# Performance work log

Measured on AMD Instinct MI355X. Metric: run time of the kernel, lower is better.

Reference implementation:

```python
import jax, jax.numpy as jnp
import numpy as np

EPS = 1e-5  # nn.BatchNorm2d default eps


def _cbs(x, w, g, b, m, v):
    # Conv(k=1, bias=False) + BatchNorm2d(inference) + SiLU
    y = jnp.einsum('bchw,oc->bohw', x, w)
    s = (g * jax.lax.rsqrt(v + EPS))[None, :, None, None]
    y = (y - m[None, :, None, None]) * s + b[None, :, None, None]
    return y * jax.nn.sigmoid(y)


def setup_inputs():
    key = jax.random.key(0)
    B, D, H, W = 1, 256, 80, 80
    C = D // 2
    ks = jax.random.split(key, 20)
    r = lambda i, shape, sc=1.0: jax.random.normal(ks[i], shape, dtype=jnp.float32) * sc
    oC, oD = jnp.ones((C,), jnp.float32), jnp.ones((D,), jnp.float32)
    zC, zD = jnp.zeros((C,), jnp.float32), jnp.zeros((D,), jnp.float32)
    return {
        'x': r(0, (B, D, H, W)),
        'w1': r(1, (C, D), 0.05), 'g1': oC, 'b1': zC, 'm1': zC, 'v1': oC,
        'w2': r(2, (D, C), 0.05), 'g2': oD, 'b2': zD, 'm2': zD, 'v2': oD,
        'w3': r(3, (D, C), 0.05), 'g3': oD, 'b3': zD, 'm3': zD, 'v3': oD,
        'wq': r(4, (C, C), 0.05), 'bq': r(5, (C,), 0.01),
        'wk': r(6, (C, C), 0.05), 'bk': r(7, (C,), 0.01),
        'wv': r(8, (C, C), 0.05), 'bv': r(9, (C,), 0.01),
        'wp': r(10, (C, C), 0.05), 'bp': r(11, (C,), 0.01),
        'rel_h': r(12, (1, C, H, 1)), 'rel_w': r(13, (1, C, 1, W)),
        'ef_h': r(14, (1, C, H, 1)), 'ef_w': r(15, (1, C, 1, W)),
    }


def reference(x, w1, g1, b1, m1, v1, w2, g2, b2, m2, v2, w3, g3, b3, m3, v3,
              wq, bq, wk, bk, wv, bv, wp, bp, rel_h, rel_w, ef_h, ef_w):
    x1 = _cbs(x, w1, g1, b1, m1, v1)            # [B, C, H, W]
    B, C, H, W = x1.shape
    HW = H * W
    proj = lambda w, b: (jnp.einsum('bchw,oc->bohw', x1, w)
                         + b[None, :, None, None]).reshape(B, C, HW)
    q = proj(wq, bq)
    k = proj(wk, bk)
    v = proj(wv, bv)
    p = proj(wp, bp)
    # content-content + content-position attention branch
    cp = (rel_h + rel_w).reshape(C, HW)          # [C, HW]
    cc = jnp.einsum('bci,bcj->bij', q, k)        # [B, HW, HW]
    cpos = jnp.einsum('ci,bcj->bij', cp, q)      # [B, HW, HW]
    attn = jax.nn.softmax(cc + cpos, axis=-1)
    # out1[b,c,i] = sum_j v[b,c,j] * attn[b,i,j]  (bmm(v, attn^T))
    out1 = jnp.einsum('bcj,bij->bci', v, attn).reshape(B, C, H, W)
    # extra positional branch (valid because B == 1)
    ef = (ef_h + ef_w).reshape(B, C, HW)         # [1, C, HW]
    ce = jnp.einsum('bci,bcj->bij', p, ef)       # [B, HW, HW]
    eng = jax.nn.softmax(ce, axis=-1)
    out2 = jnp.einsum('bcj,bij->bci', ef, eng).reshape(B, C, H, W)
    return x + _cbs(out1, w2, g2, b2, m2, v2) + _cbs(out2, w3, g3, b3, m3, v3)
```

## Files before the change

### kernel.cpp

```cpp
#include <hip/hip_runtime.h>


typedef unsigned short u16;
typedef __attribute__((ext_vector_type(8))) short bf16x8;
typedef __attribute__((ext_vector_type(4))) float f32x4;
typedef __attribute__((ext_vector_type(4))) unsigned int u32x4;

#define HW 6400
#define BN_EPS 1e-5f

__device__ __forceinline__ u16 f2b(float f) {
  unsigned u = __float_as_uint(f);
  u += 0x7fffu + ((u >> 16) & 1u);
  return (u16)(u >> 16);
}
__device__ __forceinline__ unsigned pack2(float a, float b) {
  return (unsigned)f2b(a) | ((unsigned)f2b(b) << 16);
}
__device__ __forceinline__ f32x4 MFMA(bf16x8 a, bf16x8 b, f32x4 c) {
  return __builtin_amdgcn_mfma_f32_16x16x32_bf16(a, b, c, 0, 0, 0);
}
__device__ __forceinline__ float silu_f(float y) {
  return y / (1.0f + __expf(-y));
}
__device__ __forceinline__ bf16x8 pack8(f32x4 lo, f32x4 hi, float sc) {
  union { bf16x8 v; uint4 u; } r;
  r.u.x = pack2(lo[0] * sc, lo[1] * sc);
  r.u.y = pack2(lo[2] * sc, lo[3] * sc);
  r.u.z = pack2(hi[0] * sc, hi[1] * sc);
  r.u.w = pack2(hi[2] * sc, hi[3] * sc);
  return r.v;
}
__device__ __forceinline__ void gload_lds16(const u16* src, u16* dst) {
  __builtin_amdgcn_global_load_lds(
      (const __attribute__((address_space(1))) void*)src,
      (__attribute__((address_space(3))) void*)dst, 16, 0, 0);
}

__global__ void prep_all(
    const float* __restrict__ rel_h, const float* __restrict__ rel_w,
    const float* __restrict__ ef_h, const float* __restrict__ ef_w,
    const float* __restrict__ w1, const float* __restrict__ g1, const float* __restrict__ b1,
    const float* __restrict__ m1, const float* __restrict__ v1,
    const float* __restrict__ w2, const float* __restrict__ g2, const float* __restrict__ b2,
    const float* __restrict__ m2, const float* __restrict__ v2,
    const float* __restrict__ w3, const float* __restrict__ g3, const float* __restrict__ b3,
    const float* __restrict__ m3, const float* __restrict__ v3,
    const float* __restrict__ wq, const float* __restrict__ bq,
    const float* __restrict__ wk, const float* __restrict__ bk,
    const float* __restrict__ wv, const float* __restrict__ bv,
    const float* __restrict__ wp, const float* __restrict__ bp,
    u16* __restrict__ LT,
    u16* __restrict__ w1b, float* __restrict__ b1e,
    u16* __restrict__ Wcat, float* __restrict__ bcat,
    u16* __restrict__ w2b, float* __restrict__ b2e,
    u16* __restrict__ w3b, float* __restrict__ b3e,
    u16* __restrict__ efhT, u16* __restrict__ efwT,
    u16* __restrict__ efhB, u16* __restrict__ efwB,
    u16* __restrict__ expA, u16* __restrict__ expB,
    float* __restrict__ lbuf)
{
  const int b = blockIdx.x;
  const int t = threadIdx.x;
  if (b < 80) {
    const int h = b;
    const int c0 = (t & 63) * 2;
    const float rh0 = rel_h[c0 * 80 + h], rh1 = rel_h[(c0 + 1) * 80 + h];
    for (int wcol = (t >> 6); wcol < 80; wcol += 4) {
      const int i = h * 80 + wcol;
      float rw0 = rel_w[c0 * 80 + wcol], rw1 = rel_w[(c0 + 1) * 80 + wcol];
      *(unsigned*)&LT[(size_t)i * 256 + 128 + c0] = pack2(rh0 + rw0, rh1 + rw1);
    }
  } else if (b < 144) {
    const int tid = (b - 80) * 256 + t;
    const int stride = 64 * 256;
    for (int idx = tid; idx < 128 * 256; idx += stride) {
      int o = idx >> 8;
      float s = g1[o] * rsqrtf(v1[o] + BN_EPS);
      w1b[idx] = f2b(w1[idx] * s);
    }
    for (int idx = tid; idx < 128; idx += stride) {
      float s = g1[idx] * rsqrtf(v1[idx] + BN_EPS);
      b1e[idx] = b1[idx] - m1[idx] * s;
    }
    for (int idx = tid; idx < 4 * 128 * 128; idx += stride) {
      int which = idx >> 14, r = idx & 16383;
      const float* src = which == 0 ? wq : which == 1 ? wk : which == 2 ? wv : wp;
      Wcat[idx] = f2b(src[r]);
    }
    for (int idx = tid; idx < 512; idx += stride) {
      int which = idx >> 7, r = idx & 127;
      const float* src = which == 0 ? bq : which == 1 ? bk : which == 2 ? bv : bp;
      bcat[idx] = src[r];
    }
    for (int idx = tid; idx < 256 * 128; idx += stride) {
      int o = idx >> 7;
      float s2 = g2[o] * rsqrtf(v2[o] + BN_EPS);
      w2b[idx] = f2b(w2[idx] * s2);
      float s3 = g3[o] * rsqrtf(v3[o] + BN_EPS);
      w3b[idx] = f2b(w3[idx] * s3);
    }
    for (int idx = tid; idx < 256; idx += stride) {
      float s2 = g2[idx] * rsqrtf(v2[idx] + BN_EPS);
      b2e[idx] = b2[idx] - m2[idx] * s2;
      float s3 = g3[idx] * rsqrtf(v3[idx] + BN_EPS);
      b3e[idx] = b3[idx] - m3[idx] * s3;
    }
    for (int idx = tid; idx < 80 * 128; idx += stride) {
      int hj = idx >> 7, c = idx & 127;
      efhT[idx] = f2b(ef_h[c * 80 + hj]);
      efwT[idx] = f2b(ef_w[c * 80 + hj]);
    }
    for (int idx = tid; idx < 128 * 96; idx += stride) {
      int c = idx / 96, hj = idx % 96;
      efhB[idx] = hj < 80 ? f2b(ef_h[c * 80 + hj]) : (u16)0;
      efwB[idx] = hj < 80 ? f2b(ef_w[c * 80 + hj]) : (u16)0;
    }
  } else {
    const int tid = (b - 144) * 256 + t;
    const int stride = 32 * 256;
    for (int idx = tid; idx < HW / 4; idx += stride)
      ((f32x4*)lbuf)[idx] = (f32x4){0.f, 0.f, 0.f, 0.f};
    for (int idx = tid; idx < HW * 96 / 8; idx += stride) {
      ((u32x4*)expA)[idx] = (u32x4){0, 0, 0, 0};
      ((u32x4*)expB)[idx] = (u32x4){0, 0, 0, 0};
    }
  }
}

__global__ __launch_bounds__(64) void front_k(
    const float* __restrict__ x,
    const u16* __restrict__ w1b, const float* __restrict__ b1e,
    const u16* __restrict__ Wcat, const float* __restrict__ bcat,
    u16* __restrict__ LT, u16* __restrict__ RT, u16* __restrict__ Vv,
    u16* __restrict__ pT)
{
  __shared__ __align__(16) float xs[16][260];
  __shared__ __align__(16) u16 tr[16][136];
  const int t = threadIdx.x, lane = t & 63, jl = lane & 15, q = lane >> 4;
  const int i0 = blockIdx.x * 16;

#pragma unroll
  for (int p = 0; p < 16; ++p) {
    const int ch = p * 16 + (lane >> 2);
    const int ii = (lane & 3) * 4;
    f32x4 v = *(const f32x4*)(x + (size_t)ch * HW + i0 + ii);
    xs[ii][ch] = v[0]; xs[ii + 1][ch] = v[1];
    xs[ii + 2][ch] = v[2]; xs[ii + 3][ch] = v[3];
  }
  __syncthreads();

  bf16x8 afr[8];
#pragma unroll
  for (int ks = 0; ks < 8; ++ks) {
    f32x4 va = *(const f32x4*)&xs[jl][ks * 32 + q * 8];
    f32x4 vb = *(const f32x4*)&xs[jl][ks * 32 + q * 8 + 4];
    afr[ks] = pack8(va, vb, 1.0f);
  }
  f32x4 acc[8];
#pragma unroll
  for (int nf = 0; nf < 8; ++nf) acc[nf] = (f32x4){0.f, 0.f, 0.f, 0.f};
#pragma unroll
  for (int ks = 0; ks < 8; ++ks)
#pragma unroll
    for (int nf = 0; nf < 8; ++nf) {
      bf16x8 b = *(const bf16x8*)(w1b + (size_t)(nf * 16 + jl) * 256 + ks * 32 + q * 8);
      acc[nf] = MFMA(afr[ks], b, acc[nf]);
    }
#pragma unroll
  for (int nf = 0; nf < 8; ++nf) {
    const int c = nf * 16 + jl;
    const float bias = b1e[c];
#pragma unroll
    for (int r = 0; r < 4; ++r)
      tr[q * 4 + r][c] = f2b(silu_f(acc[nf][r] + bias));
  }
  __syncthreads();
  bf16x8 xa[4];
#pragma unroll
  for (int ks = 0; ks < 4; ++ks)
    xa[ks] = *(const bf16x8*)&tr[jl][ks * 32 + q * 8];

#pragma unroll
  for (int nc = 0; nc < 4; ++nc) {
    f32x4 a2[8];
#pragma unroll
    for (int nf = 0; nf < 8; ++nf) a2[nf] = (f32x4){0.f, 0.f, 0.f, 0.f};
#pragma unroll
    for (int ks = 0; ks < 4; ++ks)
#pragma unroll
      for (int nf = 0; nf < 8; ++nf) {
        bf16x8 b = *(const bf16x8*)(Wcat + (size_t)(nc * 128 + nf * 16 + jl) * 128 + ks * 32 + q * 8);
        a2[nf] = MFMA(xa[ks], b, a2[nf]);
      }
    if (nc == 2) {
#pragma unroll
      for (int nf = 0; nf < 8; ++nf) {
        const int c = nf * 16 + jl;
        const float bias = bcat[256 + c];
        uint2 pk;
        pk.x = pack2(a2[nf][0] + bias, a2[nf][1] + bias);
        pk.y = pack2(a2[nf][2] + bias, a2[nf][3] + bias);
        *(uint2*)(Vv + (size_t)c * HW + i0 + q * 4) = pk;
      }
    } else {
      __syncthreads();
#pragma unroll
      for (int nf = 0; nf < 8; ++nf) {
        const int c = nf * 16 + jl;
        const float bias = bcat[nc * 128 + c];
#pragma unroll
        for (int r = 0; r < 4; ++r)
          tr[q * 4 + r][c] = f2b(a2[nf][r] + bias);
      }
      __syncthreads();
#pragma unroll
      for (int r = 0; r < 16; ++r) {
        unsigned val = *(const unsigned*)&tr[r][lane * 2];
        const size_t row = (size_t)(i0 + r);
        if (nc == 0) {
          *(unsigned*)(LT + row * 256 + lane * 2) = val;
          *(unsigned*)(RT + row * 256 + 128 + lane * 2) = val;
        } else if (nc == 1) {
          *(unsigned*)(RT + row * 256 + lane * 2) = val;
        } else {
          *(unsigned*)(pT + row * 128 + lane * 2) = val;
        }
      }
    }
  }
}

__global__ __launch_bounds__(256) void sep2a(
    const u16* __restrict__ pT,
    const u16* __restrict__ efhT,
    const u16* __restrict__ efwT,
    u16* __restrict__ expA, u16* __restrict__ expB,
    float* __restrict__ sA, float* __restrict__ sB)
{
  const int t = threadIdx.x, lane = t & 63, w = t >> 6, jl = lane & 15, q = lane >> 4;
  const int i0w = blockIdx.x * 128 + w * 32;

  bf16x8 pfr[2][4];
#pragma unroll
  for (int mt = 0; mt < 2; ++mt)
#pragma unroll
    for (int l = 0; l < 4; ++l)
      pfr[mt][l] = *(const bf16x8*)(pT + (size_t)(i0w + mt * 16 + jl) * 128 + l * 32 + q * 8);

  f32x4 sa[5][2], sb[5][2];
#pragma unroll
  for (int nf = 0; nf < 5; ++nf)
#pragma unroll
    for (int mt = 0; mt < 2; ++mt) {
      sa[nf][mt] = (f32x4){0.f, 0.f, 0.f, 0.f};
      sb[nf][mt] = (f32x4){0.f, 0.f, 0.f, 0.f};
    }
#pragma unroll
  for (int nf = 0; nf < 5; ++nf) {
    const int row = nf * 16 + jl;
#pragma unroll
    for (int l = 0; l < 4; ++l) {
      bf16x8 eh = *(const bf16x8*)(efhT + (size_t)row * 128 + l * 32 + q * 8);
      bf16x8 ew = *(const bf16x8*)(efwT + (size_t)row * 128 + l * 32 + q * 8);
      sa[nf][0] = MFMA(eh, pfr[0][l], sa[nf][0]);
      sa[nf][1] = MFMA(eh, pfr[1][l], sa[nf][1]);
      sb[nf][0] = MFMA(ew, pfr[0][l], sb[nf][0]);
      sb[nf][1] = MFMA(ew, pfr[1][l], sb[nf][1]);
    }
  }
#pragma unroll
  for (int mt = 0; mt < 2; ++mt) {
    const int i = i0w + mt * 16 + jl;
    float ra = 0.f, rb = 0.f;
#pragma unroll
    for (int nf = 0; nf < 5; ++nf) {
      float ea[4], eb[4];
#pragma unroll
      for (int r = 0; r < 4; ++r) {
        ea[r] = __expf(sa[nf][mt][r]); ra += ea[r];
        eb[r] = __expf(sb[nf][mt][r]); rb += eb[r];
      }
      uint2 pa, pb;
      pa.x = pack2(ea[0], ea[1]); pa.y = pack2(ea[2], ea[3]);
      pb.x = pack2(eb[0], eb[1]); pb.y = pack2(eb[2], eb[3]);
      *(uint2*)(expA + (size_t)i * 96 + nf * 16 + q * 4) = pa;
      *(uint2*)(expB + (size_t)i * 96 + nf * 16 + q * 4) = pb;
    }
    ra += __shfl_xor(ra, 16); ra += __shfl_xor(ra, 32);
    rb += __shfl_xor(rb, 16); rb += __shfl_xor(rb, 32);
    if (lane < 16) { sA[i] = ra; sB[i] = rb; }
  }
}

__global__ __launch_bounds__(512, 2) void fused_attn(
    const u16* __restrict__ LT,
    const u16* __restrict__ RT,
    const u16* __restrict__ Vv,
    float* __restrict__ Opart,
    float* __restrict__ lv)
{
  __shared__ __align__(1024) u16 Rs[2][128 * 128];
  __shared__ __align__(1024) u16 Ts[2][64 * 128];
  const int t = threadIdx.x, lane = t & 63, w = t >> 6, jl = lane & 15, q = lane >> 4;
  const int bid = blockIdx.x;
  const int jp = bid / 50, it = bid % 50;
  const int wi = w & 1, wj = w >> 1;
  const int i0w = it * 128 + wi * 64;
  u16* Tw = Ts[wi];

  bf16x8 afr[4][8];
#pragma unroll
  for (int mt = 0; mt < 4; ++mt)
#pragma unroll
    for (int l = 0; l < 8; ++l)
      afr[mt][l] = *(const bf16x8*)(LT + (size_t)(i0w + mt * 16 + jl) * 256 + l * 32 + q * 8);

  f32x4 o[4][2];
#pragma unroll
  for (int mt = 0; mt < 4; ++mt)
#pragma unroll
    for (int cf = 0; cf < 2; ++cf) o[mt][cf] = (f32x4){0.f, 0.f, 0.f, 0.f};
  float lacc[4] = {0.f, 0.f, 0.f, 0.f};

  auto stage = [&](int jj) {
#pragma unroll
    for (int k = 0; k < 8; ++k) {
      const int b = k >> 2, cl = k & 3;
      const int cc = w * 4 + cl;
      const int jr = cc * 4 + (lane >> 4);
      const int cp = lane & 15;
      const int ch = (cp & ~7) | ((cp ^ jr) & 7);
      gload_lds16(RT + (size_t)(jj + jr) * 256 + b * 128 + ch * 8,
                  Rs[b] + (cc << 9));
    }
  };

  stage(jp * 640);

  for (int stp = 0; stp < 5; ++stp) {
    const int jj = jp * 640 + stp * 128;

    f32x4 s[2][4];
#pragma unroll
    for (int nf = 0; nf < 2; ++nf)
#pragma unroll
      for (int mt = 0; mt < 4; ++mt) s[nf][mt] = (f32x4){0.f, 0.f, 0.f, 0.f};

    __syncthreads();

#pragma unroll
    for (int h = 0; h < 2; ++h)
#pragma unroll
      for (int nf = 0; nf < 2; ++nf) {
        const int row = wj * 32 + nf * 16 + jl;
#pragma unroll
        for (int l = 0; l < 4; ++l) {
          const int ch = (l * 4 + q) ^ (jl & 7);
          bf16x8 b = *(const bf16x8*)(Rs[h] + row * 128 + ch * 8);
          s[nf][0] = MFMA(b, afr[0][h * 4 + l], s[nf][0]);
          s[nf][1] = MFMA(b, afr[1][h * 4 + l], s[nf][1]);
          s[nf][2] = MFMA(b, afr[2][h * 4 + l], s[nf][2]);
          s[nf][3] = MFMA(b, afr[3][h * 4 + l], s[nf][3]);
        }
      }
    __syncthreads();
    if (stp < 4) stage(jj + 128);

#pragma unroll
    for (int nf = 0; nf < 2; ++nf)
#pragma unroll
      for (int mt = 0; mt < 4; ++mt)
#pragma unroll
        for (int r = 0; r < 4; ++r) {
          float p = __expf(s[nf][mt][r]);
          s[nf][mt][r] = p;
          lacc[mt] += p;
        }

#pragma unroll
    for (int mt = 0; mt < 4; ++mt)
#pragma unroll
      for (int nf = 0; nf < 2; ++nf) {
        const int row = mt * 16 + jl;
        const int cs = (wj * 8 + nf * 4 + q) ^ ((jl & 7) << 2);
        uint2 pk;
        pk.x = pack2(s[nf][mt][0], s[nf][mt][1]);
        pk.y = pack2(s[nf][mt][2], s[nf][mt][3]);
        *(uint2*)(Tw + row * 128 + cs * 4) = pk;
      }
    __syncthreads();

#pragma unroll
    for (int ks2 = 0; ks2 < 4; ++ks2) {
      bf16x8 bv0 = *(const bf16x8*)(Vv + (size_t)(wj * 32 + jl) * HW + jj + ks2 * 32 + q * 8);
      bf16x8 bv1 = *(const bf16x8*)(Vv + (size_t)(wj * 32 + 16 + jl) * HW + jj + ks2 * 32 + q * 8);
      const int cb = (ks2 * 8 + q * 2) ^ ((jl & 7) << 2);
#pragma unroll
      for (int mt = 0; mt < 4; ++mt) {
        bf16x8 pa = *(const bf16x8*)(Tw + (mt * 16 + jl) * 128 + cb * 4);
        o[mt][0] = MFMA(pa, bv0, o[mt][0]);
        o[mt][1] = MFMA(pa, bv1, o[mt][1]);
      }
    }
  }

#pragma unroll
  for (int mt = 0; mt < 4; ++mt) {
    float rsum = lacc[mt];
    rsum += __shfl_xor(rsum, 16);
    rsum += __shfl_xor(rsum, 32);
    if (lane < 16)
      atomicAdd(&lv[i0w + mt * 16 + jl], rsum);
  }
#pragma unroll
  for (int mt = 0; mt < 4; ++mt) {
    const int ib = i0w + mt * 16 + q * 4;
#pragma unroll
    for (int cf = 0; cf < 2; ++cf) {
      const int c = wj * 32 + cf * 16 + jl;
#pragma unroll
      for (int r = 0; r < 4; ++r)
        Opart[((size_t)(ib + r) * 10 + jp) * 128 + c] = o[mt][cf][r];
    }
  }
}

__global__ __launch_bounds__(256) void final2(
    const u16* __restrict__ expA, const u16* __restrict__ expB,
    const float* __restrict__ sA, const float* __restrict__ sB,
    const u16* __restrict__ efhB, const u16* __restrict__ efwB,
    const float* __restrict__ Opart,
    const float* __restrict__ lv,
    const u16* __restrict__ w2b, const float* __restrict__ b2e,
    const u16* __restrict__ w3b, const float* __restrict__ b3e,
    const float* __restrict__ x, float* __restrict__ outp)
{
  __shared__ __align__(16) u16 T2[64][136];
  const int t = threadIdx.x, lane = t & 63, w = t >> 6, jl = lane & 15, q = lane >> 4;
  const int i0 = blockIdx.x * 64;
  const int nc = blockIdx.y;
  const int rowA = i0 + w * 16 + jl;

  {
    bf16x8 fa[3], fb[3];
#pragma unroll
    for (int l = 0; l < 3; ++l) {
      fa[l] = *(const bf16x8*)(expA + (size_t)rowA * 96 + l * 32 + q * 8);
      fb[l] = *(const bf16x8*)(expB + (size_t)rowA * 96 + l * 32 + q * 8);
    }
    f32x4 oU[8], oW[8];
#pragma unroll
    for (int nf = 0; nf < 8; ++nf) {
      oU[nf] = (f32x4){0.f, 0.f, 0.f, 0.f};
      oW[nf] = (f32x4){0.f, 0.f, 0.f, 0.f};
    }
#pragma unroll
    for (int l = 0; l < 3; ++l)
#pragma unroll
      for (int nf = 0; nf < 8; ++nf) {
        bf16x8 bh = *(const bf16x8*)(efhB + (size_t)(nf * 16 + jl) * 96 + l * 32 + q * 8);
        bf16x8 bw = *(const bf16x8*)(efwB + (size_t)(nf * 16 + jl) * 96 + l * 32 + q * 8);
        oU[nf] = MFMA(fa[l], bh, oU[nf]);
        oW[nf] = MFMA(fb[l], bw, oW[nf]);
      }
    const int ib = i0 + w * 16 + q * 4;
    float ia[4], iw[4];
#pragma unroll
    for (int r = 0; r < 4; ++r) {
      ia[r] = 1.0f / sA[ib + r];
      iw[r] = 1.0f / sB[ib + r];
    }
#pragma unroll
    for (int nf = 0; nf < 8; ++nf)
#pragma unroll
      for (int r = 0; r < 4; ++r)
        T2[w * 16 + q * 4 + r][nf * 16 + jl] =
            f2b(oU[nf][r] * ia[r] + oW[nf][r] * iw[r]);
  }
  __syncthreads();

  const float inv1 = 1.0f / lv[rowA];
  const float* OrBase = Opart + (size_t)rowA * 10 * 128;
  f32x4 a1[8], a2[8];
#pragma unroll
  for (int nf = 0; nf < 8; ++nf) {
    a1[nf] = (f32x4){0.f, 0.f, 0.f, 0.f};
    a2[nf] = (f32x4){0.f, 0.f, 0.f, 0.f};
  }
#pragma unroll
  for (int ks = 0; ks < 4; ++ks) {
    f32x4 s1a = (f32x4){0.f, 0.f, 0.f, 0.f};
    f32x4 s1b = (f32x4){0.f, 0.f, 0.f, 0.f};
#pragma unroll
    for (int p = 0; p < 10; ++p) {
      const float* Or = OrBase + p * 128;
      s1a += *(const f32x4*)(Or + ks * 32 + q * 8);
      s1b += *(const f32x4*)(Or + ks * 32 + q * 8 + 4);
    }
    bf16x8 fa1 = pack8(s1a, s1b, inv1);
    bf16x8 fa2 = *(const bf16x8*)&T2[w * 16 + jl][ks * 32 + q * 8];
#pragma unroll
    for (int nf = 0; nf < 8; ++nf) {
      bf16x8 b2f = *(const bf16x8*)(w2b + (size_t)(nc * 128 + nf * 16 + jl) * 128 + ks * 32 + q * 8);
      bf16x8 b3f = *(const bf16x8*)(w3b + (size_t)(nc * 128 + nf * 16 + jl) * 128 + ks * 32 + q * 8);
      a1[nf] = MFMA(fa1, b2f, a1[nf]);
      a2[nf] = MFMA(fa2, b3f, a2[nf]);
    }
  }
#pragma unroll
  for (int nf = 0; nf < 8; ++nf) {
    const int d = nc * 128 + nf * 16 + jl;
    const float bb2 = b2e[d], bb3 = b3e[d];
    const size_t base = (size_t)d * HW + i0 + w * 16 + q * 4;
    f32x4 xv = *(const f32x4*)(x + base);
    f32x4 rv;
#pragma unroll
    for (int r = 0; r < 4; ++r)
      rv[r] = xv[r] + silu_f(a1[nf][r] + bb2) + silu_f(a2[nf][r] + bb3);
    *(f32x4*)(outp + base) = rv;
  }
}

extern "C" void kernel_launch(void* const* d_in, const int* in_sizes, int n_in,
                              void* d_out, int out_size, void* d_ws, size_t ws_size,
                              hipStream_t stream)
{
  (void)in_sizes; (void)n_in; (void)out_size; (void)ws_size;
  const float* x   = (const float*)d_in[0];
  const float* w1  = (const float*)d_in[1];
  const float* g1  = (const float*)d_in[2];
  const float* b1  = (const float*)d_in[3];
  const float* m1  = (const float*)d_in[4];
  const float* v1  = (const float*)d_in[5];
  const float* w2  = (const float*)d_in[6];
  const float* g2  = (const float*)d_in[7];
  const float* b2  = (const float*)d_in[8];
  const float* m2  = (const float*)d_in[9];
  const float* v2  = (const float*)d_in[10];
  const float* w3  = (const float*)d_in[11];
  const float* g3  = (const float*)d_in[12];
  const float* b3  = (const float*)d_in[13];
  const float* m3  = (const float*)d_in[14];
  const float* v3  = (const float*)d_in[15];
  const float* wq  = (const float*)d_in[16];
  const float* bq  = (const float*)d_in[17];
  const float* wk  = (const float*)d_in[18];
  const float* bk  = (const float*)d_in[19];
  const float* wv  = (const float*)d_in[20];
  const float* bv  = (const float*)d_in[21];
  const float* wp  = (const float*)d_in[22];
  const float* bp  = (const float*)d_in[23];
  const float* rel_h = (const float*)d_in[24];
  const float* rel_w = (const float*)d_in[25];
  const float* ef_h  = (const float*)d_in[26];
  const float* ef_w  = (const float*)d_in[27];
  float* outp = (float*)d_out;

  char* ws = (char*)d_ws;
  size_t off = 0;
  auto alloc = [&](size_t bytes) -> void* {
    void* p = ws + off;
    off += (bytes + 511) & ~(size_t)511;
    return p;
  };
  u16* LT    = (u16*)alloc((size_t)HW * 256 * 2);
  u16* RT    = (u16*)alloc((size_t)HW * 256 * 2);
  u16* pT    = (u16*)alloc((size_t)HW * 128 * 2);
  u16* Vv    = (u16*)alloc((size_t)HW * 128 * 2);
  float* Opart = (float*)alloc((size_t)HW * 10 * 128 * 4);
  float* lbuf  = (float*)alloc((size_t)HW * 4);
  u16* w1b   = (u16*)alloc(128 * 256 * 2);
  float* b1e = (float*)alloc(128 * 4);
  u16* Wcat  = (u16*)alloc(512 * 128 * 2);
  float* bcat = (float*)alloc(512 * 4);
  u16* w2b   = (u16*)alloc(256 * 128 * 2);
  float* b2e = (float*)alloc(256 * 4);
  u16* w3b   = (u16*)alloc(256 * 128 * 2);
  float* b3e = (float*)alloc(256 * 4);
  u16* efhT  = (u16*)alloc(80 * 128 * 2);
  u16* efwT  = (u16*)alloc(80 * 128 * 2);
  u16* efhB  = (u16*)alloc(128 * 96 * 2);
  u16* efwB  = (u16*)alloc(128 * 96 * 2);
  u16* expA  = (u16*)alloc((size_t)HW * 96 * 2);
  u16* expB  = (u16*)alloc((size_t)HW * 96 * 2);
  float* sA  = (float*)alloc(HW * 4);
  float* sB  = (float*)alloc(HW * 4);

  prep_all<<<176, 256, 0, stream>>>(rel_h, rel_w, ef_h, ef_w,
                                    w1, g1, b1, m1, v1, w2, g2, b2, m2, v2,
                                    w3, g3, b3, m3, v3, wq, bq, wk, bk, wv, bv, wp, bp,
                                    LT, w1b, b1e, Wcat, bcat, w2b, b2e, w3b, b3e,
                                    efhT, efwT, efhB, efwB, expA, expB, lbuf);
  front_k<<<400, 64, 0, stream>>>(x, w1b, b1e, Wcat, bcat, LT, RT, Vv, pT);
  sep2a<<<50, 256, 0, stream>>>(pT, efhT, efwT, expA, expB, sA, sB);
  fused_attn<<<500, 512, 0, stream>>>(LT, RT, Vv, Opart, lbuf);
  final2<<<dim3(100, 2), 256, 0, stream>>>(expA, expB, sA, sB, efhB, efwB,
                                           Opart, lbuf, w2b, b2e, w3b, b3e,
                                           x, outp);
}
```

Baseline: 245.2 us.

## Fuse ef-softmax kernel into final2 and spread front_k across four waves

Removes the sep2a kernel and its expA/expB/sA/sB global buffers: final2 now computes the p·ef scores, exponentials and row sums into shared memory for its 64-row tile before using them. This drops one launch, the zeroing of the exp buffers in prep_all, and a global write/read round trip. In exchange, the softmax work is repeated for each of the two blockIdx.y halves. Separately, front_k goes from one to four waves per block, each wave owning a quarter of the output columns and the load/store rows, to raise parallelism inside each block.

```diff
diff --git a/kernel.cpp b/kernel.cpp
--- a/kernel.cpp
+++ b/kernel.cpp
@@ -57,7 +57,6 @@
     u16* __restrict__ w3b, float* __restrict__ b3e,
     u16* __restrict__ efhT, u16* __restrict__ efwT,
     u16* __restrict__ efhB, u16* __restrict__ efwB,
-    u16* __restrict__ expA, u16* __restrict__ expB,
     float* __restrict__ lbuf)
 {
   const int b = blockIdx.x;
@@ -121,14 +120,10 @@
     const int stride = 32 * 256;
     for (int idx = tid; idx < HW / 4; idx += stride)
       ((f32x4*)lbuf)[idx] = (f32x4){0.f, 0.f, 0.f, 0.f};
-    for (int idx = tid; idx < HW * 96 / 8; idx += stride) {
-      ((u32x4*)expA)[idx] = (u32x4){0, 0, 0, 0};
-      ((u32x4*)expB)[idx] = (u32x4){0, 0, 0, 0};
-    }
-  }
-}
-
-__global__ __launch_bounds__(64) void front_k(
+  }
+}
+
+__global__ __launch_bounds__(256) void front_k(
     const float* __restrict__ x,
     const u16* __restrict__ w1b, const float* __restrict__ b1e,
     const u16* __restrict__ Wcat, const float* __restrict__ bcat,
@@ -137,11 +132,12 @@
 {
   __shared__ __align__(16) float xs[16][260];
   __shared__ __align__(16) u16 tr[16][136];
-  const int t = threadIdx.x, lane = t & 63, jl = lane & 15, q = lane >> 4;
+  const int t = threadIdx.x, lane = t & 63, w = t >> 6, jl = lane & 15, q = lane >> 4;
   const int i0 = blockIdx.x * 16;
 
 #pragma unroll
-  for (int p = 0; p < 16; ++p) {
+  for (int pp = 0; pp < 4; ++pp) {
+    const int p = w * 4 + pp;
     const int ch = p * 16 + (lane >> 2);
     const int ii = (lane & 3) * 4;
     f32x4 v = *(const f32x4*)(x + (size_t)ch * HW + i0 + ii);
@@ -157,23 +153,24 @@
     f32x4 vb = *(const f32x4*)&xs[jl][ks * 32 + q * 8 + 4];
     afr[ks] = pack8(va, vb, 1.0f);
   }
-  f32x4 acc[8];
-#pragma unroll
-  for (int nf = 0; nf < 8; ++nf) acc[nf] = (f32x4){0.f, 0.f, 0.f, 0.f};
+  f32x4 acc[2];
+#pragma unroll
+  for (int nn = 0; nn < 2; ++nn) acc[nn] = (f32x4){0.f, 0.f, 0.f, 0.f};
 #pragma unroll
   for (int ks = 0; ks < 8; ++ks)
 #pragma unroll
-    for (int nf = 0; nf < 8; ++nf) {
+    for (int nn = 0; nn < 2; ++nn) {
+      const int nf = w * 2 + nn;
       bf16x8 b = *(const bf16x8*)(w1b + (size_t)(nf * 16 + jl) * 256 + ks * 32 + q * 8);
-      acc[nf] = MFMA(afr[ks], b, acc[nf]);
-    }
-#pragma unroll
-  for (int nf = 0; nf < 8; ++nf) {
-    const int c = nf * 16 + jl;
+      acc[nn] = MFMA(afr[ks], b, acc[nn]);
+    }
+#pragma unroll
+  for (int nn = 0; nn < 2; ++nn) {
+    const int c = (w * 2 + nn) * 16 + jl;
     const float bias = b1e[c];
 #pragma unroll
     for (int r = 0; r < 4; ++r)
-      tr[q * 4 + r][c] = f2b(silu_f(acc[nf][r] + bias));
+      tr[q * 4 + r][c] = f2b(silu_f(acc[nn][r] + bias));
   }
   __syncthreads();
   bf16x8 xa[4];
@@ -183,39 +180,41 @@
 
 #pragma unroll
   for (int nc = 0; nc < 4; ++nc) {
-    f32x4 a2[8];
-#pragma unroll
-    for (int nf = 0; nf < 8; ++nf) a2[nf] = (f32x4){0.f, 0.f, 0.f, 0.f};
+    f32x4 a2[2];
+#pragma unroll
+    for (int nn = 0; nn < 2; ++nn) a2[nn] = (f32x4){0.f, 0.f, 0.f, 0.f};
 #pragma unroll
     for (int ks = 0; ks < 4; ++ks)
 #pragma unroll
-      for (int nf = 0; nf < 8; ++nf) {
+      for (int nn = 0; nn < 2; ++nn) {
+        const int nf = w * 2 + nn;
         bf16x8 b = *(const bf16x8*)(Wcat + (size_t)(nc * 128 + nf * 16 + jl) * 128 + ks * 32 + q * 8);
-        a2[nf] = MFMA(xa[ks], b, a2[nf]);
+        a2[nn] = MFMA(xa[ks], b, a2[nn]);
       }
     if (nc == 2) {
 #pragma unroll
-      for (int nf = 0; nf < 8; ++nf) {
-        const int c = nf * 16 + jl;
+      for (int nn = 0; nn < 2; ++nn) {
+        const int c = (w * 2 + nn) * 16 + jl;
         const float bias = bcat[256 + c];
         uint2 pk;
-        pk.x = pack2(a2[nf][0] + bias, a2[nf][1] + bias);
-        pk.y = pack2(a2[nf][2] + bias, a2[nf][3] + bias);
+        pk.x = pack2(a2[nn][0] + bias, a2[nn][1] + bias);
+        pk.y = pack2(a2[nn][2] + bias, a2[nn][3] + bias);
         *(uint2*)(Vv + (size_t)c * HW + i0 + q * 4) = pk;
       }
     } else {
       __syncthreads();
 #pragma unroll
-      for (int nf = 0; nf < 8; ++nf) {
-        const int c = nf * 16 + jl;
+      for (int nn = 0; nn < 2; ++nn) {
+        const int c = (w * 2 + nn) * 16 + jl;
         const float bias = bcat[nc * 128 + c];
 #pragma unroll
         for (int r = 0; r < 4; ++r)
-          tr[q * 4 + r][c] = f2b(a2[nf][r] + bias);
+          tr[q * 4 + r][c] = f2b(a2[nn][r] + bias);
       }
       __syncthreads();
 #pragma unroll
-      for (int r = 0; r < 16; ++r) {
+      for (int rr = 0; rr < 4; ++rr) {
+        const int r = w * 4 + rr;
         unsigned val = *(const unsigned*)&tr[r][lane * 2];
         const size_t row = (size_t)(i0 + r);
         if (nc == 0) {
@@ -228,68 +227,6 @@
         }
       }
     }
-  }
-}
-
-__global__ __launch_bounds__(256) void sep2a(
-    const u16* __restrict__ pT,
-    const u16* __restrict__ efhT,
-    const u16* __restrict__ efwT,
-    u16* __restrict__ expA, u16* __restrict__ expB,
-    float* __restrict__ sA, float* __restrict__ sB)
-{
-  const int t = threadIdx.x, lane = t & 63, w = t >> 6, jl = lane & 15, q = lane >> 4;
-  const int i0w = blockIdx.x * 128 + w * 32;
-
-  bf16x8 pfr[2][4];
-#pragma unroll
-  for (int mt = 0; mt < 2; ++mt)
-#pragma unroll
-    for (int l = 0; l < 4; ++l)
-      pfr[mt][l] = *(const bf16x8*)(pT + (size_t)(i0w + mt * 16 + jl) * 128 + l * 32 + q * 8);
-
-  f32x4 sa[5][2], sb[5][2];
-#pragma unroll
-  for (int nf = 0; nf < 5; ++nf)
-#pragma unroll
-    for (int mt = 0; mt < 2; ++mt) {
-      sa[nf][mt] = (f32x4){0.f, 0.f, 0.f, 0.f};
-      sb[nf][mt] = (f32x4){0.f, 0.f, 0.f, 0.f};
-    }
-#pragma unroll
-  for (int nf = 0; nf < 5; ++nf) {
-    const int row = nf * 16 + jl;
-#pragma unroll
-    for (int l = 0; l < 4; ++l) {
-      bf16x8 eh = *(const bf16x8*)(efhT + (size_t)row * 128 + l * 32 + q * 8);
-      bf16x8 ew = *(const bf16x8*)(efwT + (size_t)row * 128 + l * 32 + q * 8);
-      sa[nf][0] = MFMA(eh, pfr[0][l], sa[nf][0]);
-      sa[nf][1] = MFMA(eh, pfr[1][l], sa[nf][1]);
-      sb[nf][0] = MFMA(ew, pfr[0][l], sb[nf][0]);
-      sb[nf][1] = MFMA(ew, pfr[1][l], sb[nf][1]);
-    }
-  }
-#pragma unroll
-  for (int mt = 0; mt < 2; ++mt) {
-    const int i = i0w + mt * 16 + jl;
-    float ra = 0.f, rb = 0.f;
-#pragma unroll
-    for (int nf = 0; nf < 5; ++nf) {
-      float ea[4], eb[4];
-#pragma unroll
-      for (int r = 0; r < 4; ++r) {
-        ea[r] = __expf(sa[nf][mt][r]); ra += ea[r];
-        eb[r] = __expf(sb[nf][mt][r]); rb += eb[r];
-      }
-      uint2 pa, pb;
-      pa.x = pack2(ea[0], ea[1]); pa.y = pack2(ea[2], ea[3]);
-      pb.x = pack2(eb[0], eb[1]); pb.y = pack2(eb[2], eb[3]);
-      *(uint2*)(expA + (size_t)i * 96 + nf * 16 + q * 4) = pa;
-      *(uint2*)(expB + (size_t)i * 96 + nf * 16 + q * 4) = pb;
-    }
-    ra += __shfl_xor(ra, 16); ra += __shfl_xor(ra, 32);
-    rb += __shfl_xor(rb, 16); rb += __shfl_xor(rb, 32);
-    if (lane < 16) { sA[i] = ra; sB[i] = rb; }
   }
 }
 
@@ -427,8 +364,8 @@
 }
 
 __global__ __launch_bounds__(256) void final2(
-    const u16* __restrict__ expA, const u16* __restrict__ expB,
-    const float* __restrict__ sA, const float* __restrict__ sB,
+    const u16* __restrict__ pT,
+    const u16* __restrict__ efhT, const u16* __restrict__ efwT,
     const u16* __restrict__ efhB, const u16* __restrict__ efwB,
     const float* __restrict__ Opart,
     const float* __restrict__ lv,
@@ -436,18 +373,67 @@
     const u16* __restrict__ w3b, const float* __restrict__ b3e,
     const float* __restrict__ x, float* __restrict__ outp)
 {
+  __shared__ __align__(16) u16 eAs[64][104];
+  __shared__ __align__(16) u16 eBs[64][104];
+  __shared__ float sAL[64], sBL[64];
   __shared__ __align__(16) u16 T2[64][136];
   const int t = threadIdx.x, lane = t & 63, w = t >> 6, jl = lane & 15, q = lane >> 4;
   const int i0 = blockIdx.x * 64;
   const int nc = blockIdx.y;
   const int rowA = i0 + w * 16 + jl;
+  const int iloc = w * 16 + jl;
+
+  {
+    bf16x8 pfr[4];
+#pragma unroll
+    for (int l = 0; l < 4; ++l)
+      pfr[l] = *(const bf16x8*)(pT + (size_t)rowA * 128 + l * 32 + q * 8);
+    f32x4 sa[5], sb[5];
+#pragma unroll
+    for (int nf = 0; nf < 5; ++nf) {
+      sa[nf] = (f32x4){0.f, 0.f, 0.f, 0.f};
+      sb[nf] = (f32x4){0.f, 0.f, 0.f, 0.f};
+    }
+#pragma unroll
+    for (int nf = 0; nf < 5; ++nf) {
+      const int row = nf * 16 + jl;
+#pragma unroll
+      for (int l = 0; l < 4; ++l) {
+        bf16x8 eh = *(const bf16x8*)(efhT + (size_t)row * 128 + l * 32 + q * 8);
+        bf16x8 ew = *(const bf16x8*)(efwT + (size_t)row * 128 + l * 32 + q * 8);
+        sa[nf] = MFMA(eh, pfr[l], sa[nf]);
+        sb[nf] = MFMA(ew, pfr[l], sb[nf]);
+      }
+    }
+    float ra = 0.f, rb = 0.f;
+#pragma unroll
+    for (int nf = 0; nf < 5; ++nf) {
+      float ea[4], eb[4];
+#pragma unroll
+      for (int r = 0; r < 4; ++r) {
+        ea[r] = __expf(sa[nf][r]); ra += ea[r];
+        eb[r] = __expf(sb[nf][r]); rb += eb[r];
+      }
+      uint2 pa, pb;
+      pa.x = pack2(ea[0], ea[1]); pa.y = pack2(ea[2], ea[3]);
+      pb.x = pack2(eb[0], eb[1]); pb.y = pack2(eb[2], eb[3]);
+      *(uint2*)&eAs[iloc][nf * 16 + q * 4] = pa;
+      *(uint2*)&eBs[iloc][nf * 16 + q * 4] = pb;
+    }
+    *(uint2*)&eAs[iloc][80 + q * 4] = (uint2){0u, 0u};
+    *(uint2*)&eBs[iloc][80 + q * 4] = (uint2){0u, 0u};
+    ra += __shfl_xor(ra, 16); ra += __shfl_xor(ra, 32);
+    rb += __shfl_xor(rb, 16); rb += __shfl_xor(rb, 32);
+    if (lane < 16) { sAL[iloc] = ra; sBL[iloc] = rb; }
+  }
+  __syncthreads();
 
   {
     bf16x8 fa[3], fb[3];
 #pragma unroll
     for (int l = 0; l < 3; ++l) {
-      fa[l] = *(const bf16x8*)(expA + (size_t)rowA * 96 + l * 32 + q * 8);
-      fb[l] = *(const bf16x8*)(expB + (size_t)rowA * 96 + l * 32 + q * 8);
+      fa[l] = *(const bf16x8*)&eAs[iloc][l * 32 + q * 8];
+      fb[l] = *(const bf16x8*)&eBs[iloc][l * 32 + q * 8];
     }
     f32x4 oU[8], oW[8];
 #pragma unroll
@@ -464,12 +450,11 @@
         oU[nf] = MFMA(fa[l], bh, oU[nf]);
         oW[nf] = MFMA(fb[l], bw, oW[nf]);
       }
-    const int ib = i0 + w * 16 + q * 4;
     float ia[4], iw[4];
 #pragma unroll
     for (int r = 0; r < 4; ++r) {
-      ia[r] = 1.0f / sA[ib + r];
-      iw[r] = 1.0f / sB[ib + r];
+      ia[r] = 1.0f / sAL[w * 16 + q * 4 + r];
+      iw[r] = 1.0f / sBL[w * 16 + q * 4 + r];
     }
 #pragma unroll
     for (int nf = 0; nf < 8; ++nf)
@@ -582,20 +567,15 @@
   u16* efwT  = (u16*)alloc(80 * 128 * 2);
   u16* efhB  = (u16*)alloc(128 * 96 * 2);
   u16* efwB  = (u16*)alloc(128 * 96 * 2);
-  u16* expA  = (u16*)alloc((size_t)HW * 96 * 2);
-  u16* expB  = (u16*)alloc((size_t)HW * 96 * 2);
-  float* sA  = (float*)alloc(HW * 4);
-  float* sB  = (float*)alloc(HW * 4);
 
   prep_all<<<176, 256, 0, stream>>>(rel_h, rel_w, ef_h, ef_w,
                                     w1, g1, b1, m1, v1, w2, g2, b2, m2, v2,
                                     w3, g3, b3, m3, v3, wq, bq, wk, bk, wv, bv, wp, bp,
                                     LT, w1b, b1e, Wcat, bcat, w2b, b2e, w3b, b3e,
-                                    efhT, efwT, efhB, efwB, expA, expB, lbuf);
-  front_k<<<400, 64, 0, stream>>>(x, w1b, b1e, Wcat, bcat, LT, RT, Vv, pT);
-  sep2a<<<50, 256, 0, stream>>>(pT, efhT, efwT, expA, expB, sA, sB);
+                                    efhT, efwT, efhB, efwB, lbuf);
+  front_k<<<400, 256, 0, stream>>>(x, w1b, b1e, Wcat, bcat, LT, RT, Vv, pT);
   fused_attn<<<500, 512, 0, stream>>>(LT, RT, Vv, Opart, lbuf);
-  final2<<<dim3(100, 2), 256, 0, stream>>>(expA, expB, sA, sB, efhB, efwB,
+  final2<<<dim3(100, 2), 256, 0, stream>>>(pT, efhT, efwT, efhB, efwB,
                                            Opart, lbuf, w2b, b2e, w3b, b3e,
                                            x, outp);
 }
```

After: 240.8 us. No clear change (-1.8%).
